# Performance work log

Hardware: AMD Instinct MI355X
Metric: run time of the kernel (lower is better)

Reference implementation:

```python
import jax, jax.numpy as jnp
import numpy as np

N_NODES = 100000
N_EDGES = 300000
D = 256
EPS = 1e-5
ALPHA = 0.5  # residual_alpha


def setup_inputs() -> dict:
    key = jax.random.key(0)
    ks = jax.random.split(key, 6)
    x = jax.random.normal(ks[0], (N_NODES, D), dtype=jnp.float32)
    edge_index = jax.random.randint(ks[1], (2, N_EDGES), 0, N_NODES, dtype=jnp.int32)
    edge_weight = jax.random.uniform(ks[2], (N_EDGES,), dtype=jnp.float32)
    # GCNConv parameters (glorot-ish weight, bias)
    W = jax.random.normal(ks[3], (D, D), dtype=jnp.float32) / np.float32(np.sqrt(D))
    b = 0.01 * jax.random.normal(ks[4], (D,), dtype=jnp.float32)
    # LayerNorm parameters
    gamma = jnp.ones((D,), dtype=jnp.float32)
    beta = jnp.zeros((D,), dtype=jnp.float32)
    return {"x": x, "edge_index": edge_index, "edge_weight": edge_weight,
            "W": W, "b": b, "gamma": gamma, "beta": beta}


def gcn_residual(x, edge_index, edge_weight, W, b, gamma, beta):
    src, dst = edge_index[0], edge_index[1]
    # linear transform first (PyG GCNConv order)
    h = x @ W  # [N, D]
    # gcn_norm with added self-loops (self-loop weight = 1)
    deg = jax.ops.segment_sum(edge_weight, dst, num_segments=N_NODES) + 1.0  # [N]
    dinv = jax.lax.rsqrt(deg)
    norm = dinv[src] * edge_weight * dinv[dst]  # [E]
    # message + aggregate (scatter-add over destination nodes)
    agg = jax.ops.segment_sum(norm[:, None] * h[src], dst, num_segments=N_NODES)
    agg = agg + (dinv * dinv)[:, None] * h  # self-loop contribution
    h = agg + b
    # LayerNorm over feature dim
    mu = jnp.mean(h, axis=-1, keepdims=True)
    var = jnp.mean(jnp.square(h - mu), axis=-1, keepdims=True)
    h = (h - mu) * jax.lax.rsqrt(var + EPS) * gamma + beta
    # dropout p=0.0 -> identity; weighted residual; relu
    h = ALPHA * h + (1.0 - ALPHA) * x
    return jax.nn.relu(h)


def reference(x, edge_index, edge_weight, W, b, gamma, beta):
    return gcn_residual(x, edge_index, edge_weight, W, b, gamma, beta)
```

## Files before the change

kernel.cpp:

```cpp
#include <hip/hip_runtime.h>


#define NN 100000
#define NE 300000
#define DD 256
#define NB 391
#define GMB 782

typedef __attribute__((ext_vector_type(8))) short short8;
typedef __attribute__((ext_vector_type(4))) short short4v;
typedef __attribute__((ext_vector_type(4))) float f32x4;
typedef __attribute__((ext_vector_type(4))) unsigned short u16x4;

static __device__ __forceinline__ short f2bf(float f) {
  union { float f; unsigned u; } a; a.f = f;
  unsigned r = a.u + 0x7fffu + ((a.u >> 16) & 1u);
  return (short)(r >> 16);
}

static __device__ __forceinline__ float4 bf4_to_f4(u16x4 v) {
  float4 r;
  r.x = __uint_as_float((unsigned)v[0] << 16);
  r.y = __uint_as_float((unsigned)v[1] << 16);
  r.z = __uint_as_float((unsigned)v[2] << 16);
  r.w = __uint_as_float((unsigned)v[3] << 16);
  return r;
}

__global__ __launch_bounds__(256) void k_init(float* __restrict__ dv,
                                              int* __restrict__ cnt) {
  int i = blockIdx.x * 256 + threadIdx.x;
  if (i < NN) { dv[i] = 0.0f; cnt[i] = 0; }
}

__global__ __launch_bounds__(256) void k_hist(const int* __restrict__ ei,
                                              const float* __restrict__ ew,
                                              float* __restrict__ dv,
                                              int* __restrict__ cnt) {
  int e = blockIdx.x * 256 + threadIdx.x;
  if (e < NE) {
    int d = ei[NE + e];
    atomicAdd(&dv[d], ew[e]);
    atomicAdd(&cnt[d], 1);
  }
}

__global__ __launch_bounds__(256) void k_dinv(float* __restrict__ dv) {
  int i = blockIdx.x * 256 + threadIdx.x;
  if (i < NN) dv[i] = rsqrtf(dv[i] + 1.0f);
}

__global__ __launch_bounds__(256) void k_scan1(const int* __restrict__ cnt,
                                               int* __restrict__ off,
                                               int* __restrict__ bsum) {
  __shared__ int tmp[256];
  int t = threadIdx.x;
  int i = blockIdx.x * 256 + t;
  int v = (i < NN) ? cnt[i] : 0;
  tmp[t] = v;
  __syncthreads();
  for (int o = 1; o < 256; o <<= 1) {
    int u = (t >= o) ? tmp[t - o] : 0;
    __syncthreads();
    tmp[t] += u;
    __syncthreads();
  }
  if (i < NN) off[i] = tmp[t] - v;
  if (t == 255) bsum[blockIdx.x] = tmp[t];
}

__global__ __launch_bounds__(512) void k_scan2(int* __restrict__ bsum) {
  __shared__ int tmp[512];
  int t = threadIdx.x;
  int v = (t < NB) ? bsum[t] : 0;
  tmp[t] = v;
  __syncthreads();
  for (int o = 1; o < 512; o <<= 1) {
    int u = (t >= o) ? tmp[t - o] : 0;
    __syncthreads();
    tmp[t] += u;
    __syncthreads();
  }
  bsum[t] = tmp[t] - v;
}

__global__ __launch_bounds__(256) void k_scan3(int* __restrict__ off,
                                               const int* __restrict__ bsum,
                                               int* __restrict__ cur) {
  int i = blockIdx.x * 256 + threadIdx.x;
  if (i < NN) {
    int o = off[i] + bsum[i >> 8];
    off[i] = o;
    cur[i] = o;
  }
}

__global__ __launch_bounds__(256) void k_place(const int* __restrict__ ei,
                                               const float* __restrict__ ew,
                                               const float* __restrict__ dv,
                                               int* __restrict__ cur,
                                               int2* __restrict__ elist) {
  int e = blockIdx.x * 256 + threadIdx.x;
  if (e >= NE) return;
  int s = ei[e];
  int d = ei[NE + e];
  float c = dv[s] * ew[e] * dv[d];
  int pos = atomicAdd(&cur[d], 1);
  elist[pos] = make_int2(s, __float_as_int(c));
}

__global__ __launch_bounds__(256) void k_wprep(const float* __restrict__ W,
                                               short* __restrict__ Wf) {
  int idx = blockIdx.x * 256 + threadIdx.x;
  int k = idx >> 6;
  int c4 = idx & 63;
  const float4 v = *(const float4*)(W + k * 256 + c4 * 4);
  float vv[4] = {v.x, v.y, v.z, v.w};
#pragma unroll
  for (int i = 0; i < 4; ++i) {
    int c = c4 * 4 + i;
    int di = ((k >> 5) * 16 + (c >> 4)) * 512 + ((c & 15) + ((k >> 3) & 3) * 16) * 8 + (k & 7);
    Wf[di] = f2bf(vv[i]);
  }
}

__global__ __launch_bounds__(512) void k_gemm(const float* __restrict__ x,
                                              const short* __restrict__ Wf,
                                              short* __restrict__ h) {
  __shared__ short As[128 * 256];

  const int t = threadIdx.x;
  const int lane = t & 63;
  const int wid = t >> 6;
  const int row0 = blockIdx.x * 128;
  const int wrow = (wid >> 2) * 64;
  const int wcg = (wid & 3) * 4;

#pragma unroll
  for (int i = 0; i < 8; ++i) {
    int p = i * 512 + t;
    int r = p >> 5;
    int kp = p & 31;
    int grow = row0 + r;
    float4 v0 = make_float4(0.f, 0.f, 0.f, 0.f);
    float4 v1 = v0;
    if (grow < NN) {
      const float* src = x + (size_t)grow * 256 + kp * 8;
      v0 = *(const float4*)(src);
      v1 = *(const float4*)(src + 4);
    }
    short8 s;
    s[0] = f2bf(v0.x); s[1] = f2bf(v0.y); s[2] = f2bf(v0.z); s[3] = f2bf(v0.w);
    s[4] = f2bf(v1.x); s[5] = f2bf(v1.y); s[6] = f2bf(v1.z); s[7] = f2bf(v1.w);
    int byte = (r * 512 + kp * 16) ^ ((r & 7) << 4);
    *(short8*)((char*)As + byte) = s;
  }
  __syncthreads();

  f32x4 acc[4][4];
#pragma unroll
  for (int m = 0; m < 4; ++m)
#pragma unroll
    for (int n = 0; n < 4; ++n) acc[m][n] = (f32x4)0.0f;

#pragma unroll
  for (int ks = 0; ks < 8; ++ks) {
    short8 afrag[4];
    short8 bfrag[4];
#pragma unroll
    for (int m = 0; m < 4; ++m) {
      int r = wrow + m * 16 + (lane & 15);
      int byte = (r * 512 + ks * 64 + (lane >> 4) * 16) ^ ((r & 7) << 4);
      afrag[m] = *(short8*)((char*)As + byte);
    }
#pragma unroll
    for (int n = 0; n < 4; ++n) {
      size_t fi = (size_t)(ks * 16 + wcg + n) * 64 + lane;
      bfrag[n] = *(const short8*)(Wf + fi * 8);
    }
#pragma unroll
    for (int m = 0; m < 4; ++m)
#pragma unroll
      for (int n = 0; n < 4; ++n)
        acc[m][n] = __builtin_amdgcn_mfma_f32_16x16x32_bf16(
            afrag[m], bfrag[n], acc[m][n], 0, 0, 0);
  }

#pragma unroll
  for (int m = 0; m < 4; ++m) {
    int rbase = wrow + m * 16 + (lane >> 4) * 4;
#pragma unroll
    for (int j = 0; j < 4; ++j) {
      int grow = row0 + rbase + j;
      if (grow >= NN) continue;
#pragma unroll
      for (int n = 0; n < 4; ++n) {
        int c = (wcg + n) * 16 + (lane & 15);
        h[(size_t)grow * 256 + c] = f2bf(acc[m][n][j]);
      }
    }
  }
}

__global__ __launch_bounds__(256) void k_agg(const short* __restrict__ h,
                                             const float* __restrict__ dv,
                                             const int* __restrict__ cnt,
                                             const int* __restrict__ off,
                                             const int2* __restrict__ elist,
                                             const float* __restrict__ x,
                                             const float* __restrict__ b,
                                             const float* __restrict__ gamma,
                                             const float* __restrict__ beta,
                                             float* __restrict__ out) {
  int node = blockIdx.x * 4 + (threadIdx.x >> 6);
  if (node >= NN) return;
  int lane = threadIdx.x & 63;

  const float di = dv[node];
  const float d2 = di * di;
  float4 acc = bf4_to_f4(((const u16x4*)(h + (size_t)node * 256))[lane]);
  acc.x *= d2; acc.y *= d2; acc.z *= d2; acc.w *= d2;

  const int n = cnt[node];
  const int st = off[node];
  if (n > 0) {
    int2 rec = elist[st];
    for (int j = 0; j < n; ++j) {
      int2 nrec = (j + 1 < n) ? elist[st + j + 1] : rec;
      float c = __int_as_float(rec.y);
      float4 v = bf4_to_f4(((const u16x4*)(h + (size_t)rec.x * 256))[lane]);
      acc.x += c * v.x; acc.y += c * v.y; acc.z += c * v.z; acc.w += c * v.w;
      rec = nrec;
    }
  }

  const float4 bb = *(const float4*)(b + lane * 4);
  acc.x += bb.x; acc.y += bb.y; acc.z += bb.z; acc.w += bb.w;

  float s = acc.x + acc.y + acc.z + acc.w;
  float ss = acc.x * acc.x + acc.y * acc.y + acc.z * acc.z + acc.w * acc.w;
#pragma unroll
  for (int o = 32; o > 0; o >>= 1) {
    s += __shfl_xor(s, o);
    ss += __shfl_xor(ss, o);
  }
  const float mu = s * (1.0f / 256.0f);
  const float var = ss * (1.0f / 256.0f) - mu * mu;
  const float inv = rsqrtf(var + 1e-5f);

  const float4 g = *(const float4*)(gamma + lane * 4);
  const float4 be = *(const float4*)(beta + lane * 4);
  const float4 xx = *(const float4*)(x + (size_t)node * 256 + lane * 4);
  float4 r;
  r.x = 0.5f * ((acc.x - mu) * inv * g.x + be.x) + 0.5f * xx.x;
  r.y = 0.5f * ((acc.y - mu) * inv * g.y + be.y) + 0.5f * xx.y;
  r.z = 0.5f * ((acc.z - mu) * inv * g.z + be.z) + 0.5f * xx.z;
  r.w = 0.5f * ((acc.w - mu) * inv * g.w + be.w) + 0.5f * xx.w;
  r.x = fmaxf(r.x, 0.0f); r.y = fmaxf(r.y, 0.0f);
  r.z = fmaxf(r.z, 0.0f); r.w = fmaxf(r.w, 0.0f);
  *(float4*)(out + (size_t)node * 256 + lane * 4) = r;
}

extern "C" void kernel_launch(void* const* d_in, const int* in_sizes, int n_in,
                              void* d_out, int out_size, void* d_ws, size_t ws_size,
                              hipStream_t stream) {
  const float* x     = (const float*)d_in[0];
  const int*   ei    = (const int*)d_in[1];
  const float* ew    = (const float*)d_in[2];
  const float* W     = (const float*)d_in[3];
  const float* b     = (const float*)d_in[4];
  const float* gamma = (const float*)d_in[5];
  const float* beta  = (const float*)d_in[6];
  float* out = (float*)d_out;

  short* h   = (short*)d_ws;
  float* dv  = (float*)(h + (size_t)NN * DD);
  int*   cnt = (int*)(dv + NN);
  int*   off = cnt + NN;
  int*   cur = off + NN;
  int*   bsum = cur + NN;
  int2*  elist = (int2*)(bsum + 512);
  short* Wf  = (short*)(elist + NE);

  k_init<<<NB, 256, 0, stream>>>(dv, cnt);
  k_hist<<<(NE + 255) / 256, 256, 0, stream>>>(ei, ew, dv, cnt);
  k_dinv<<<NB, 256, 0, stream>>>(dv);
  k_scan1<<<NB, 256, 0, stream>>>(cnt, off, bsum);
  k_scan2<<<1, 512, 0, stream>>>(bsum);
  k_scan3<<<NB, 256, 0, stream>>>(off, bsum, cur);
  k_place<<<(NE + 255) / 256, 256, 0, stream>>>(ei, ew, dv, cur, elist);

  k_wprep<<<64, 256, 0, stream>>>(W, Wf);
  k_gemm<<<GMB, 512, 0, stream>>>(x, Wf, h);

  k_agg<<<(NN + 3) / 4, 256, 0, stream>>>(h, dv, cnt, off, elist, x, b, gamma, beta, out);
}
```

Before: 181.7 us.

## Shrink GEMM tile, swap MFMA operands for vector stores, widen agg gathers

The GEMM tile drops from 128 to 64 rows per block, which doubles the grid and halves shared memory. The MFMA operands are swapped (W as A, x as B) so each lane holds four consecutive output columns and can write h with packed 8-byte stores instead of scattered 2-byte stores. All global x loads are also issued before any bf16 conversion. The aggregation kernel now uses 32 lanes per node with 16-byte bf16 gathers and unrolls the edge loop by two, aiming for more memory-level parallelism. In exchange, W fragments are reused across fewer rows, and the per-lane register count in the aggregation kernel goes up.

```diff
diff --git a/kernel.cpp b/kernel.cpp
--- a/kernel.cpp
+++ b/kernel.cpp
@@ -5,7 +5,7 @@
 #define NE 300000
 #define DD 256
 #define NB 391
-#define GMB 782
+#define GMB 1563
 
 typedef __attribute__((ext_vector_type(8))) short short8;
 typedef __attribute__((ext_vector_type(4))) short short4v;
@@ -18,13 +18,8 @@
   return (short)(r >> 16);
 }
 
-static __device__ __forceinline__ float4 bf4_to_f4(u16x4 v) {
-  float4 r;
-  r.x = __uint_as_float((unsigned)v[0] << 16);
-  r.y = __uint_as_float((unsigned)v[1] << 16);
-  r.z = __uint_as_float((unsigned)v[2] << 16);
-  r.w = __uint_as_float((unsigned)v[3] << 16);
-  return r;
+static __device__ __forceinline__ float bf2f(short s) {
+  return __uint_as_float((unsigned)(unsigned short)s << 16);
 }
 
 __global__ __launch_bounds__(256) void k_init(float* __restrict__ dv,
@@ -127,76 +122,86 @@
 __global__ __launch_bounds__(512) void k_gemm(const float* __restrict__ x,
                                               const short* __restrict__ Wf,
                                               short* __restrict__ h) {
-  __shared__ short As[128 * 256];
+  __shared__ short As[64 * 256];
 
   const int t = threadIdx.x;
   const int lane = t & 63;
   const int wid = t >> 6;
-  const int row0 = blockIdx.x * 128;
-  const int wrow = (wid >> 2) * 64;
-  const int wcg = (wid & 3) * 4;
-
-#pragma unroll
-  for (int i = 0; i < 8; ++i) {
+  const int row0 = blockIdx.x * 64;
+  const int wrow = (wid >> 2) * 32;
+  const int wstrip = (wid & 3);
+
+  float4 va[4], vb[4];
+#pragma unroll
+  for (int i = 0; i < 4; ++i) {
     int p = i * 512 + t;
     int r = p >> 5;
     int kp = p & 31;
     int grow = row0 + r;
-    float4 v0 = make_float4(0.f, 0.f, 0.f, 0.f);
-    float4 v1 = v0;
     if (grow < NN) {
       const float* src = x + (size_t)grow * 256 + kp * 8;
-      v0 = *(const float4*)(src);
-      v1 = *(const float4*)(src + 4);
+      va[i] = *(const float4*)(src);
+      vb[i] = *(const float4*)(src + 4);
+    } else {
+      va[i] = make_float4(0.f, 0.f, 0.f, 0.f);
+      vb[i] = va[i];
     }
+  }
+#pragma unroll
+  for (int i = 0; i < 4; ++i) {
+    int p = i * 512 + t;
+    int r = p >> 5;
+    int kp = p & 31;
     short8 s;
-    s[0] = f2bf(v0.x); s[1] = f2bf(v0.y); s[2] = f2bf(v0.z); s[3] = f2bf(v0.w);
-    s[4] = f2bf(v1.x); s[5] = f2bf(v1.y); s[6] = f2bf(v1.z); s[7] = f2bf(v1.w);
+    s[0] = f2bf(va[i].x); s[1] = f2bf(va[i].y); s[2] = f2bf(va[i].z); s[3] = f2bf(va[i].w);
+    s[4] = f2bf(vb[i].x); s[5] = f2bf(vb[i].y); s[6] = f2bf(vb[i].z); s[7] = f2bf(vb[i].w);
     int byte = (r * 512 + kp * 16) ^ ((r & 7) << 4);
     *(short8*)((char*)As + byte) = s;
   }
   __syncthreads();
 
-  f32x4 acc[4][4];
-#pragma unroll
-  for (int m = 0; m < 4; ++m)
-#pragma unroll
-    for (int n = 0; n < 4; ++n) acc[m][n] = (f32x4)0.0f;
+  f32x4 acc[4][2];
+#pragma unroll
+  for (int mc = 0; mc < 4; ++mc)
+#pragma unroll
+    for (int nr = 0; nr < 2; ++nr) acc[mc][nr] = (f32x4)0.0f;
+
+  const short* wbase = Wf + (size_t)(wstrip * 4) * 512 + lane * 8;
 
 #pragma unroll
   for (int ks = 0; ks < 8; ++ks) {
-    short8 afrag[4];
-    short8 bfrag[4];
-#pragma unroll
-    for (int m = 0; m < 4; ++m) {
-      int r = wrow + m * 16 + (lane & 15);
+    short8 bx[2];
+    short8 aw[4];
+#pragma unroll
+    for (int nr = 0; nr < 2; ++nr) {
+      int r = wrow + nr * 16 + (lane & 15);
       int byte = (r * 512 + ks * 64 + (lane >> 4) * 16) ^ ((r & 7) << 4);
-      afrag[m] = *(short8*)((char*)As + byte);
+      bx[nr] = *(short8*)((char*)As + byte);
     }
 #pragma unroll
-    for (int n = 0; n < 4; ++n) {
-      size_t fi = (size_t)(ks * 16 + wcg + n) * 64 + lane;
-      bfrag[n] = *(const short8*)(Wf + fi * 8);
-    }
-#pragma unroll
-    for (int m = 0; m < 4; ++m)
-#pragma unroll
-      for (int n = 0; n < 4; ++n)
-        acc[m][n] = __builtin_amdgcn_mfma_f32_16x16x32_bf16(
-            afrag[m], bfrag[n], acc[m][n], 0, 0, 0);
-  }
-
-#pragma unroll
-  for (int m = 0; m < 4; ++m) {
-    int rbase = wrow + m * 16 + (lane >> 4) * 4;
-#pragma unroll
-    for (int j = 0; j < 4; ++j) {
-      int grow = row0 + rbase + j;
-      if (grow >= NN) continue;
-#pragma unroll
-      for (int n = 0; n < 4; ++n) {
-        int c = (wcg + n) * 16 + (lane & 15);
-        h[(size_t)grow * 256 + c] = f2bf(acc[m][n][j]);
+    for (int mc = 0; mc < 4; ++mc)
+      aw[mc] = *(const short8*)(wbase + (size_t)(ks * 16 + mc) * 512);
+#pragma unroll
+    for (int mc = 0; mc < 4; ++mc)
+#pragma unroll
+      for (int nr = 0; nr < 2; ++nr)
+        acc[mc][nr] = __builtin_amdgcn_mfma_f32_16x16x32_bf16(
+            aw[mc], bx[nr], acc[mc][nr], 0, 0, 0);
+  }
+
+#pragma unroll
+  for (int mc = 0; mc < 4; ++mc) {
+    int cbase = wstrip * 64 + mc * 16 + 4 * (lane >> 4);
+#pragma unroll
+    for (int nr = 0; nr < 2; ++nr) {
+      int r = row0 + wrow + nr * 16 + (lane & 15);
+      if (r < NN) {
+        u16x4 s;
+        s[0] = (unsigned short)f2bf(acc[mc][nr][0]);
+        s[1] = (unsigned short)f2bf(acc[mc][nr][1]);
+        s[2] = (unsigned short)f2bf(acc[mc][nr][2]);
+        s[3] = (unsigned short)f2bf(acc[mc][nr][3]);
+        *(u16x4*)(h + (size_t)r * 256 + cbase) = s;
       }
     }
   }
@@ -212,35 +217,50 @@
                                              const float* __restrict__ gamma,
                                              const float* __restrict__ beta,
                                              float* __restrict__ out) {
-  int node = blockIdx.x * 4 + (threadIdx.x >> 6);
+  int node = (blockIdx.x * 256 + threadIdx.x) >> 5;
   if (node >= NN) return;
-  int lane = threadIdx.x & 63;
+  int q = threadIdx.x & 31;
 
   const float di = dv[node];
   const float d2 = di * di;
-  float4 acc = bf4_to_f4(((const u16x4*)(h + (size_t)node * 256))[lane]);
-  acc.x *= d2; acc.y *= d2; acc.z *= d2; acc.w *= d2;
+  short8 hv = *(const short8*)(h + (size_t)node * 256 + q * 8);
+  float a[8];
+#pragma unroll
+  for (int i = 0; i < 8; ++i) a[i] = bf2f(hv[i]) * d2;
 
   const int n = cnt[node];
   const int st = off[node];
-  if (n > 0) {
-    int2 rec = elist[st];
-    for (int j = 0; j < n; ++j) {
-      int2 nrec = (j + 1 < n) ? elist[st + j + 1] : rec;
-      float c = __int_as_float(rec.y);
-      float4 v = bf4_to_f4(((const u16x4*)(h + (size_t)rec.x * 256))[lane]);
-      acc.x += c * v.x; acc.y += c * v.y; acc.z += c * v.z; acc.w += c * v.w;
-      rec = nrec;
-    }
-  }
-
-  const float4 bb = *(const float4*)(b + lane * 4);
-  acc.x += bb.x; acc.y += bb.y; acc.z += bb.z; acc.w += bb.w;
-
-  float s = acc.x + acc.y + acc.z + acc.w;
-  float ss = acc.x * acc.x + acc.y * acc.y + acc.z * acc.z + acc.w * acc.w;
-#pragma unroll
-  for (int o = 32; o > 0; o >>= 1) {
+  int j = 0;
+  for (; j + 2 <= n; j += 2) {
+    int2 r0 = elist[st + j];
+    int2 r1 = elist[st + j + 1];
+    short8 g0 = *(const short8*)(h + (size_t)r0.x * 256 + q * 8);
+    short8 g1 = *(const short8*)(h + (size_t)r1.x * 256 + q * 8);
+    float c0 = __int_as_float(r0.y);
+    float c1 = __int_as_float(r1.y);
+#pragma unroll
+    for (int i = 0; i < 8; ++i) a[i] += c0 * bf2f(g0[i]);
+#pragma unroll
+    for (int i = 0; i < 8; ++i) a[i] += c1 * bf2f(g1[i]);
+  }
+  if (j < n) {
+    int2 r0 = elist[st + j];
+    short8 g0 = *(const short8*)(h + (size_t)r0.x * 256 + q * 8);
+    float c0 = __int_as_float(r0.y);
+#pragma unroll
+    for (int i = 0; i < 8; ++i) a[i] += c0 * bf2f(g0[i]);
+  }
+
+  const float4 b0 = *(const float4*)(b + q * 8);
+  const float4 b1 = *(const float4*)(b + q * 8 + 4);
+  a[0] += b0.x; a[1] += b0.y; a[2] += b0.z; a[3] += b0.w;
+  a[4] += b1.x; a[5] += b1.y; a[6] += b1.z; a[7] += b1.w;
+
+  float s = 0.f, ss = 0.f;
+#pragma unroll
+  for (int i = 0; i < 8; ++i) { s += a[i]; ss += a[i] * a[i]; }
+#pragma unroll
+  for (int o = 16; o > 0; o >>= 1) {
     s += __shfl_xor(s, o);
     ss += __shfl_xor(ss, o);
   }
@@ -248,17 +268,26 @@
   const float var = ss * (1.0f / 256.0f) - mu * mu;
   const float inv = rsqrtf(var + 1e-5f);
 
-  const float4 g = *(const float4*)(gamma + lane * 4);
-  const float4 be = *(const float4*)(beta + lane * 4);
-  const float4 xx = *(const float4*)(x + (size_t)node * 256 + lane * 4);
-  float4 r;
-  r.x = 0.5f * ((acc.x - mu) * inv * g.x + be.x) + 0.5f * xx.x;
-  r.y = 0.5f * ((acc.y - mu) * inv * g.y + be.y) + 0.5f * xx.y;
-  r.z = 0.5f * ((acc.z - mu) * inv * g.z + be.z) + 0.5f * xx.z;
-  r.w = 0.5f * ((acc.w - mu) * inv * g.w + be.w) + 0.5f * xx.w;
-  r.x = fmaxf(r.x, 0.0f); r.y = fmaxf(r.y, 0.0f);
-  r.z = fmaxf(r.z, 0.0f); r.w = fmaxf(r.w, 0.0f);
-  *(float4*)(out + (size_t)node * 256 + lane * 4) = r;
+  const float4 g0 = *(const float4*)(gamma + q * 8);
+  const float4 g1 = *(const float4*)(gamma + q * 8 + 4);
+  const float4 e0 = *(const float4*)(beta + q * 8);
+  const float4 e1 = *(const float4*)(beta + q * 8 + 4);
+  const float4 x0 = *(const float4*)(x + (size_t)node * 256 + q * 8);
+  const float4 x1 = *(const float4*)(x + (size_t)node * 256 + q * 8 + 4);
+
+  float4 r0, r1;
+  r0.x = fmaxf(0.5f * ((a[0] - mu) * inv * g0.x + e0.x) + 0.5f * x0.x, 0.f);
+  r0.y = fmaxf(0.5f * ((a[1] - mu) * inv * g0.y + e0.y) + 0.5f * x0.y, 0.f);
+  r0.z = fmaxf(0.5f * ((a[2] - mu) * inv * g0.z + e0.z) + 0.5f * x0.z, 0.f);
+  r0.w = fmaxf(0.5f * ((a[3] - mu) * inv * g0.w + e0.w) + 0.5f * x0.w, 0.f);
+  r1.x = fmaxf(0.5f * ((a[4] - mu) * inv * g1.x + e1.x) + 0.5f * x1.x, 0.f);
+  r1.y = fmaxf(0.5f * ((a[5] - mu) * inv * g1.y + e1.y) + 0.5f * x1.y, 0.f);
+  r1.z = fmaxf(0.5f * ((a[6] - mu) * inv * g1.z + e1.z) + 0.5f * x1.z, 0.f);
+  r1.w = fmaxf(0.5f * ((a[7] - mu) * inv * g1.w + e1.w) + 0.5f * x1.w, 0.f);
+
+  float* o = out + (size_t)node * 256 + q * 8;
+  *(float4*)(o) = r0;
+  *(float4*)(o + 4) = r1;
 }
 
 extern "C" void kernel_launch(void* const* d_in, const int* in_sizes, int n_in,
@@ -293,5 +322,5 @@
   k_wprep<<<64, 256, 0, stream>>>(W, Wf);
   k_gemm<<<GMB, 512, 0, stream>>>(x, Wf, h);
 
-  k_agg<<<(NN + 3) / 4, 256, 0, stream>>>(h, dv, cnt, off, elist, x, b, gamma, beta, out);
-}
+  k_agg<<<(NN * 32 + 255) / 256, 256, 0, stream>>>(h, dv, cnt, off, elist, x, b, gamma, beta, out);
+}
```

New measurement: 172.7 us. 5.0% less time.
